# Kernel optimization log

Hardware: AMD Instinct MI355X
Metric: run time of the kernel (lower is better)

Reference implementation:

```python
import jax, jax.numpy as jnp
import numpy as np
from math import sqrt

B, T, E, W, H = 4, 512, 1024, 64, 16
DK = E // H


def _make_position_mask(T, W):
    # mask[s, w, t] = 1 iff token s is the w-th neighbor in the window around t
    t = np.arange(T)[None, :]            # [1, T]
    w = np.arange(W)[:, None]            # [W, 1]
    idx = np.clip(t - W // 2 + w, 0, T - 1)  # [W, T] source index per (w, t)
    mask = np.zeros((T, W, T), dtype=np.float32)
    mask[idx, np.arange(W)[:, None], np.arange(T)[None, :]] = 1.0
    return jnp.asarray(mask)


def setup_inputs() -> dict:
    key = jax.random.key(0)
    ks = jax.random.split(key, 7)
    s = 1.0 / sqrt(E)
    return {
        "x": jax.random.normal(ks[0], (B, T, E), jnp.float32),
        "position_mask": _make_position_mask(T, W),
        "Wq": jax.random.normal(ks[1], (E, E), jnp.float32) * s,
        "bq": jnp.zeros((E,), jnp.float32),
        "Wv": jax.random.normal(ks[2], (E, E), jnp.float32) * s,
        "bv": jnp.zeros((E,), jnp.float32),
        "Wo": jax.random.normal(ks[3], (E, E), jnp.float32) * s,
        "bo": jnp.zeros((E,), jnp.float32),
    }


def reference(x, position_mask, Wq, bq, Wv, bv, Wo, bo):
    # gather window neighbors: attend_inputs[b,t,w,e] = sum_s x[b,s,e] * mask[s,w,t]
    attend = jnp.einsum('bse,swt->btwe', x, position_mask)  # [B,T,W,E]

    # NOTE: original splits E as (d_k, H) with d_k-major (view(..., d_k, H))
    q = (x @ Wq + bq).reshape(B, T, DK, H)                    # [B,T,DK,H]
    q = q.transpose(0, 3, 1, 2)                               # [B,H,T,DK]
    k = (attend @ Wq + bq).reshape(B, T, W, DK, H)            # key uses query_transform (as in source)
    k = k.transpose(0, 4, 1, 2, 3)                            # [B,H,T,W,DK]
    v = (attend @ Wv + bv).reshape(B, T, W, DK, H)
    v = v.transpose(0, 4, 1, 2, 3)                            # [B,H,T,W,DK]

    scores = jnp.einsum('bhtd,bhtwd->bhtw', q, k) / sqrt(E)   # scale by sqrt(E), as in source
    probs = jax.nn.softmax(scores, axis=-1)                   # softmax over window W
    out = jnp.einsum('bhtw,bhtwd->bhtd', probs, v)            # [B,H,T,DK]
    out = out.transpose(0, 2, 1, 3).reshape(B, T, E)          # merge (H, DK) H-major, as in source reshape
    return out @ Wo + bo
```

## Files before the change

### kernel.cpp

```cpp
#include <hip/hip_runtime.h>
#include <hip/hip_bf16.h>

typedef __attribute__((ext_vector_type(8))) short short8;
typedef __attribute__((ext_vector_type(4))) float f32x4;
typedef __attribute__((ext_vector_type(4))) unsigned int uint4v;

constexpr int NB = 4, NT = 512, NE = 1024, NW = 64, NH = 16, NDK = 64;
constexpr int NBT = NB * NT;
constexpr int TT = 32;
constexpr int WIN = TT + 64;

__device__ inline short f2bf(float f) {
    __hip_bfloat16 h = __float2bfloat16(f);
    return __builtin_bit_cast(short, h);
}
__device__ inline float bf2f(short s) {
    unsigned u = ((unsigned)(unsigned short)s) << 16;
    return __builtin_bit_cast(float, u);
}
__device__ inline float blo(unsigned u) { return __builtin_bit_cast(float, u << 16); }
__device__ inline float bhi(unsigned u) { return __builtin_bit_cast(float, u & 0xffff0000u); }

__global__ __launch_bounds__(256) void cast_x_kernel(const float* __restrict__ X,
                                                     short* __restrict__ Xb) {
    size_t idx = (size_t)blockIdx.x * 256 + threadIdx.x;
    const float4* p = (const float4*)(X + idx * 8);
    float4 a = p[0], b = p[1];
    short8 v;
    v[0] = f2bf(a.x); v[1] = f2bf(a.y); v[2] = f2bf(a.z); v[3] = f2bf(a.w);
    v[4] = f2bf(b.x); v[5] = f2bf(b.y); v[6] = f2bf(b.z); v[7] = f2bf(b.w);
    *(short8*)(Xb + idx * 8) = v;
}

__global__ __launch_bounds__(256) void transpose_w_kernel(const float* __restrict__ W0,
                                                          const float* __restrict__ W1,
                                                          const float* __restrict__ W2,
                                                          short* __restrict__ WTall) {
    const float* W = blockIdx.z == 0 ? W0 : (blockIdx.z == 1 ? W1 : W2);
    const bool perm = blockIdx.z < 2;
    short* WT = WTall + (size_t)blockIdx.z * NE * NE;

    __shared__ float tile[64][65];
    const int e0 = blockIdx.y * 64, j0 = blockIdx.x * 64;
    const int el = threadIdx.x & 63, grp = threadIdx.x >> 6;
    for (int i = grp; i < 64; i += 4)
        tile[i][el] = W[(size_t)(e0 + i) * NE + j0 + el];
    __syncthreads();
    for (int it = grp; it < 64; it += 4) {
        int j = j0 + it;
        int jp = perm ? ((j & 15) * 64 + (j >> 4)) : j;
        WT[(size_t)jp * NE + e0 + el] = f2bf(tile[el][it]);
    }
}

template <bool PERM_BIAS, bool OUT_BF16>
__global__ __launch_bounds__(256) void mfma_gemm_kernel(const short* __restrict__ X,
                                                        const short* __restrict__ WT,
                                                        const float* __restrict__ bias,
                                                        void* __restrict__ outv) {
    __shared__ short As[64 * 64];
    __shared__ short Bs[64 * 64];
    const int tid = threadIdx.x;
    const int lane = tid & 63, wid = tid >> 6;

    int bid = blockIdx.y * 16 + blockIdx.x;
    int swz = (bid & 7) * 64 + (bid >> 3);
    const int r0 = (swz >> 4) * 64;
    const int c0 = (swz & 15) * 64;
    const int wr = (wid >> 1) * 32, wc = (wid & 1) * 32;

    f32x4 acc[2][2];
#pragma unroll
    for (int m = 0; m < 2; m++)
#pragma unroll
        for (int n = 0; n < 2; n++) acc[m][n] = (f32x4){0.f, 0.f, 0.f, 0.f};

    short8 pfA[2], pfB[2];
    auto load_tiles = [&](int k0) {
#pragma unroll
        for (int rd = 0; rd < 2; rd++) {
            int slot = rd * 4096 + tid * 16;
            int row  = slot >> 7;
            int cp   = (slot >> 4) & 7;
            int c    = cp ^ (row & 7);
            pfA[rd] = *(const short8*)(X  + (size_t)(r0 + row) * NE + k0 + c * 8);
            pfB[rd] = *(const short8*)(WT + (size_t)(c0 + row) * NE + k0 + c * 8);
        }
    };

    load_tiles(0);
    for (int k0 = 0; k0 < NE; k0 += 64) {
        __syncthreads();
#pragma unroll
        for (int rd = 0; rd < 2; rd++) {
            int slot = rd * 4096 + tid * 16;
            *(short8*)((char*)As + slot) = pfA[rd];
            *(short8*)((char*)Bs + slot) = pfB[rd];
        }
        __syncthreads();
        if (k0 + 64 < NE) load_tiles(k0 + 64);

#pragma unroll
        for (int kk = 0; kk < 2; kk++) {
            short8 af[2], bf[2];
            const int cidx = kk * 4 + (lane >> 4);
#pragma unroll
            for (int m = 0; m < 2; m++) {
                int row = wr + m * 16 + (lane & 15);
                af[m] = *(const short8*)((char*)As + row * 128 + ((cidx ^ (row & 7)) * 16));
            }
#pragma unroll
            for (int n = 0; n < 2; n++) {
                int row = wc + n * 16 + (lane & 15);
                bf[n] = *(const short8*)((char*)Bs + row * 128 + ((cidx ^ (row & 7)) * 16));
            }
#pragma unroll
            for (int m = 0; m < 2; m++)
#pragma unroll
                for (int n = 0; n < 2; n++)
                    acc[m][n] = __builtin_amdgcn_mfma_f32_16x16x32_bf16(af[m], bf[n], acc[m][n], 0, 0, 0);
        }
    }

    short* outS = (short*)outv;
    float* outF = (float*)outv;
#pragma unroll
    for (int m = 0; m < 2; m++)
#pragma unroll
        for (int n = 0; n < 2; n++) {
            int col  = c0 + wc + n * 16 + (lane & 15);
            int bsrc = PERM_BIAS ? ((col & 63) * 16 + (col >> 6)) : col;
            float bb = bias[bsrc];
#pragma unroll
            for (int r = 0; r < 4; r++) {
                int row = r0 + wr + m * 16 + (lane >> 4) * 4 + r;
                float val = acc[m][n][r] + bb;
                if (OUT_BF16) outS[(size_t)row * NE + col] = f2bf(val);
                else          outF[(size_t)row * NE + col] = val;
            }
        }
}

__global__ __launch_bounds__(256) void attn_kernel(const short* __restrict__ Y,
                                                   const short* __restrict__ Z,
                                                   short* __restrict__ M) {
    __shared__ short KS[WIN][66];
    __shared__ short VS[WIN][66];
    __shared__ short SCb[TT][66];
    __shared__ float RED[TT][16];

    const int t0 = blockIdx.x * TT;
    const int h  = blockIdx.y;
    const int b  = blockIdx.z;
    const int tid = threadIdx.x;
    const int tl  = tid & (TT - 1);
    const int oct = tid >> 5;

    for (int idx = tid; idx < WIN * 8; idx += 256) {
        int row = idx >> 3, c = idx & 7;
        int ts = t0 - 32 + row;
        ts = ts < 0 ? 0 : (ts > NT - 1 ? NT - 1 : ts);
        size_t base = ((size_t)b * NT + ts) * NE + h * 64 + c * 8;
        uint4v ku = __builtin_bit_cast(uint4v, *(const short8*)(Y + base));
        uint4v vu = __builtin_bit_cast(uint4v, *(const short8*)(Z + base));
        unsigned* kd = (unsigned*)&KS[row][c * 8];
        unsigned* vd = (unsigned*)&VS[row][c * 8];
        kd[0] = ku[0]; kd[1] = ku[1]; kd[2] = ku[2]; kd[3] = ku[3];
        vd[0] = vu[0]; vd[1] = vu[1]; vd[2] = vu[2]; vd[3] = vu[3];
    }
    __syncthreads();

    float q[64];
    {
        const unsigned* Qr = (const unsigned*)&KS[tl + 32][0];
#pragma unroll
        for (int k2 = 0; k2 < 32; k2++) {
            unsigned u = Qr[k2];
            q[2 * k2]     = blo(u);
            q[2 * k2 + 1] = bhi(u);
        }
    }

    float sv[8];
#pragma unroll
    for (int wi = 0; wi < 8; wi++) {
        int w = oct * 8 + wi;
        const unsigned* Kr = (const unsigned*)&KS[tl + w][0];
        float acc = 0.f;
#pragma unroll
        for (int k2 = 0; k2 < 32; k2++) {
            unsigned u = Kr[k2];
            acc += q[2 * k2] * blo(u) + q[2 * k2 + 1] * bhi(u);
        }
        sv[wi] = acc * 0.03125f;
    }

    float lmax = sv[0];
#pragma unroll
    for (int wi = 1; wi < 8; wi++) lmax = fmaxf(lmax, sv[wi]);
    RED[tl][oct] = lmax;
    __syncthreads();
    float gmax = RED[tl][0];
#pragma unroll
    for (int i = 1; i < 8; i++) gmax = fmaxf(gmax, RED[tl][i]);
    float lsum = 0.f;
#pragma unroll
    for (int wi = 0; wi < 8; wi++) {
        float e = __expf(sv[wi] - gmax);
        SCb[tl][oct * 8 + wi] = f2bf(e);
        lsum += e;
    }
    RED[tl][8 + oct] = lsum;
    __syncthreads();
    float gsum = RED[tl][8];
#pragma unroll
    for (int i = 9; i < 16; i++) gsum += RED[tl][i];

    float oacc[8];
#pragma unroll
    for (int j = 0; j < 8; j++) oacc[j] = 0.f;
    for (int w = 0; w < NW; w++) {
        float p = bf2f(SCb[tl][w]);
        const unsigned* Vr = (const unsigned*)&VS[tl + w][oct * 8];
#pragma unroll
        for (int j2 = 0; j2 < 4; j2++) {
            unsigned u = Vr[j2];
            oacc[2 * j2]     += p * blo(u);
            oacc[2 * j2 + 1] += p * bhi(u);
        }
    }

    float inv = 1.0f / gsum;
    short8 ov;
#pragma unroll
    for (int j = 0; j < 8; j++) ov[j] = f2bf(oacc[j] * inv);
    size_t orow = ((size_t)b * NT + t0 + tl) * NE + h * 64 + oct * 8;
    *(short8*)(M + orow) = ov;
}

extern "C" void kernel_launch(void* const* d_in, const int* in_sizes, int n_in,
                              void* d_out, int out_size, void* d_ws, size_t ws_size,
                              hipStream_t stream) {
    const float* x  = (const float*)d_in[0];
    const float* Wq = (const float*)d_in[2];
    const float* bq = (const float*)d_in[3];
    const float* Wv = (const float*)d_in[4];
    const float* bv = (const float*)d_in[5];
    const float* Wo = (const float*)d_in[6];
    const float* bo = (const float*)d_in[7];
    float* outp = (float*)d_out;

    char* wsb = (char*)d_ws;
    short* Xb  = (short*)(wsb);
    short* WTa = (short*)(wsb + (4u << 20));
    short* Yb  = (short*)(wsb + (10u << 20));
    short* Zb  = (short*)(wsb + (14u << 20));
    short* Mb  = (short*)(wsb + (18u << 20));
    short* WTq = WTa;
    short* WTv = WTa + (size_t)NE * NE;
    short* WTo = WTv + (size_t)NE * NE;

    cast_x_kernel<<<dim3(NBT * NE / (256 * 8)), 256, 0, stream>>>(x, Xb);
    transpose_w_kernel<<<dim3(16, 16, 3), 256, 0, stream>>>(Wq, Wv, Wo, WTa);

    dim3 gg(NE / 64, NBT / 64);
    mfma_gemm_kernel<true,  true ><<<gg, 256, 0, stream>>>(Xb, WTq, bq, Yb);
    mfma_gemm_kernel<true,  true ><<<gg, 256, 0, stream>>>(Xb, WTv, bv, Zb);

    attn_kernel<<<dim3(NT / TT, NH, NB), 256, 0, stream>>>(Yb, Zb, Mb);

    mfma_gemm_kernel<false, false><<<gg, 256, 0, stream>>>(Mb, WTo, bo, (void*)outp);
}
```

Baseline: 174.6 us.

## Fuse Q and V projections into one GEMM and enlarge GEMM tiles

```diff
diff --git a/kernel.cpp b/kernel.cpp
--- a/kernel.cpp
+++ b/kernel.cpp
@@ -53,37 +53,48 @@
     }
 }
 
-template <bool PERM_BIAS, bool OUT_BF16>
+template <int BM, int BN, int LOG_GX, bool PERM_BIAS, bool OUT_BF16, bool DUAL>
 __global__ __launch_bounds__(256) void mfma_gemm_kernel(const short* __restrict__ X,
                                                         const short* __restrict__ WT,
-                                                        const float* __restrict__ bias,
-                                                        void* __restrict__ outv) {
-    __shared__ short As[64 * 64];
-    __shared__ short Bs[64 * 64];
+                                                        const float* __restrict__ bias0,
+                                                        const float* __restrict__ bias1,
+                                                        void* __restrict__ out0,
+                                                        void* __restrict__ out1) {
+    constexpr int MR = BM / 32, NR = BN / 32;
+    constexpr int RDA = BM / 32, RDB = BN / 32;
+
+    __shared__ short As[BM * 64];
+    __shared__ short Bs[BN * 64];
     const int tid = threadIdx.x;
     const int lane = tid & 63, wid = tid >> 6;
 
-    int bid = blockIdx.y * 16 + blockIdx.x;
-    int swz = (bid & 7) * 64 + (bid >> 3);
-    const int r0 = (swz >> 4) * 64;
-    const int c0 = (swz & 15) * 64;
-    const int wr = (wid >> 1) * 32, wc = (wid & 1) * 32;
-
-    f32x4 acc[2][2];
-#pragma unroll
-    for (int m = 0; m < 2; m++)
-#pragma unroll
-        for (int n = 0; n < 2; n++) acc[m][n] = (f32x4){0.f, 0.f, 0.f, 0.f};
-
-    short8 pfA[2], pfB[2];
+    const int nwg = (1 << LOG_GX) * gridDim.y;
+    const int bid = blockIdx.y * (1 << LOG_GX) + blockIdx.x;
+    const int swz = (bid & 7) * (nwg >> 3) + (bid >> 3);
+    const int r0 = (swz >> LOG_GX) * BM;
+    const int c0 = (swz & ((1 << LOG_GX) - 1)) * BN;
+    const int wr = (wid >> 1) * (BM / 2), wc = (wid & 1) * (BN / 2);
+
+    f32x4 acc[MR][NR];
+#pragma unroll
+    for (int m = 0; m < MR; m++)
+#pragma unroll
+        for (int n = 0; n < NR; n++) acc[m][n] = (f32x4){0.f, 0.f, 0.f, 0.f};
+
+    short8 pfA[RDA], pfB[RDB];
     auto load_tiles = [&](int k0) {
 #pragma unroll
-        for (int rd = 0; rd < 2; rd++) {
+        for (int rd = 0; rd < RDA; rd++) {
             int slot = rd * 4096 + tid * 16;
             int row  = slot >> 7;
-            int cp   = (slot >> 4) & 7;
-            int c    = cp ^ (row & 7);
-            pfA[rd] = *(const short8*)(X  + (size_t)(r0 + row) * NE + k0 + c * 8);
+            int c    = ((slot >> 4) & 7) ^ (row & 7);
+            pfA[rd] = *(const short8*)(X + (size_t)(r0 + row) * NE + k0 + c * 8);
+        }
+#pragma unroll
+        for (int rd = 0; rd < RDB; rd++) {
+            int slot = rd * 4096 + tid * 16;
+            int row  = slot >> 7;
+            int c    = ((slot >> 4) & 7) ^ (row & 7);
             pfB[rd] = *(const short8*)(WT + (size_t)(c0 + row) * NE + k0 + c * 8);
         }
     };
@@ -92,51 +103,55 @@
     for (int k0 = 0; k0 < NE; k0 += 64) {
         __syncthreads();
 #pragma unroll
-        for (int rd = 0; rd < 2; rd++) {
-            int slot = rd * 4096 + tid * 16;
-            *(short8*)((char*)As + slot) = pfA[rd];
-            *(short8*)((char*)Bs + slot) = pfB[rd];
-        }
+        for (int rd = 0; rd < RDA; rd++)
+            *(short8*)((char*)As + rd * 4096 + tid * 16) = pfA[rd];
+#pragma unroll
+        for (int rd = 0; rd < RDB; rd++)
+            *(short8*)((char*)Bs + rd * 4096 + tid * 16) = pfB[rd];
         __syncthreads();
         if (k0 + 64 < NE) load_tiles(k0 + 64);
 
 #pragma unroll
         for (int kk = 0; kk < 2; kk++) {
-            short8 af[2], bf[2];
+            short8 af[MR], bf[NR];
             const int cidx = kk * 4 + (lane >> 4);
 #pragma unroll
-            for (int m = 0; m < 2; m++) {
+            for (int m = 0; m < MR; m++) {
                 int row = wr + m * 16 + (lane & 15);
                 af[m] = *(const short8*)((char*)As + row * 128 + ((cidx ^ (row & 7)) * 16));
             }
 #pragma unroll
-            for (int n = 0; n < 2; n++) {
+            for (int n = 0; n < NR; n++) {
                 int row = wc + n * 16 + (lane & 15);
                 bf[n] = *(const short8*)((char*)Bs + row * 128 + ((cidx ^ (row & 7)) * 16));
             }
 #pragma unroll
-            for (int m = 0; m < 2; m++)
-#pragma unroll
-                for (int n = 0; n < 2; n++)
+            for (int m = 0; m < MR; m++)
+#pragma unroll
+                for (int n = 0; n < NR; n++)
                     acc[m][n] = __builtin_amdgcn_mfma_f32_16x16x32_bf16(af[m], bf[n], acc[m][n], 0, 0, 0);
         }
     }
 
+    const float* bias = bias0;
+    void* outv = out0;
+    int cbase = c0;
+    if (DUAL && c0 >= NE) { bias = bias1; outv = out1; cbase = c0 - NE; }
     short* outS = (short*)outv;
     float* outF = (float*)outv;
 #pragma unroll
-    for (int m = 0; m < 2; m++)
-#pragma unroll
-        for (int n = 0; n < 2; n++) {
-            int col  = c0 + wc + n * 16 + (lane & 15);
-            int bsrc = PERM_BIAS ? ((col & 63) * 16 + (col >> 6)) : col;
+    for (int m = 0; m < MR; m++)
+#pragma unroll
+        for (int n = 0; n < NR; n++) {
+            int lc   = cbase + wc + n * 16 + (lane & 15);
+            int bsrc = PERM_BIAS ? ((lc & 63) * 16 + (lc >> 6)) : lc;
             float bb = bias[bsrc];
 #pragma unroll
             for (int r = 0; r < 4; r++) {
                 int row = r0 + wr + m * 16 + (lane >> 4) * 4 + r;
                 float val = acc[m][n][r] + bb;
-                if (OUT_BF16) outS[(size_t)row * NE + col] = f2bf(val);
-                else          outF[(size_t)row * NE + col] = val;
+                if (OUT_BF16) outS[(size_t)row * NE + lc] = f2bf(val);
+                else          outF[(size_t)row * NE + lc] = val;
             }
         }
 }
@@ -256,18 +271,16 @@
     short* Yb  = (short*)(wsb + (10u << 20));
     short* Zb  = (short*)(wsb + (14u << 20));
     short* Mb  = (short*)(wsb + (18u << 20));
-    short* WTq = WTa;
-    short* WTv = WTa + (size_t)NE * NE;
-    short* WTo = WTv + (size_t)NE * NE;
+    short* WTo = WTa + 2 * (size_t)NE * NE;
 
     cast_x_kernel<<<dim3(NBT * NE / (256 * 8)), 256, 0, stream>>>(x, Xb);
     transpose_w_kernel<<<dim3(16, 16, 3), 256, 0, stream>>>(Wq, Wv, Wo, WTa);
 
-    dim3 gg(NE / 64, NBT / 64);
-    mfma_gemm_kernel<true,  true ><<<gg, 256, 0, stream>>>(Xb, WTq, bq, Yb);
-    mfma_gemm_kernel<true,  true ><<<gg, 256, 0, stream>>>(Xb, WTv, bv, Zb);
+    mfma_gemm_kernel<128, 128, 4, true, true, true>
+        <<<dim3(2 * NE / 128, NBT / 128), 256, 0, stream>>>(Xb, WTa, bq, bv, Yb, Zb);
 
     attn_kernel<<<dim3(NT / TT, NH, NB), 256, 0, stream>>>(Yb, Zb, Mb);
 
-    mfma_gemm_kernel<false, false><<<gg, 256, 0, stream>>>(Mb, WTo, bo, (void*)outp);
-}
+    mfma_gemm_kernel<64, 128, 3, false, false, false>
+        <<<dim3(NE / 128, NBT / 64), 256, 0, stream>>>(Mb, WTo, bo, nullptr, (void*)outp, nullptr);
+}
```

Result: faster. 168.8 us (-3.3%).

## Fuse all stages into one persistent cooperative kernel with grid barriers

Applied to the files above, without the earlier changes.

```diff
diff --git a/kernel.cpp b/kernel.cpp
--- a/kernel.cpp
+++ b/kernel.cpp
@@ -3,239 +3,326 @@
 
 typedef __attribute__((ext_vector_type(8))) short short8;
 typedef __attribute__((ext_vector_type(4))) float f32x4;
-typedef __attribute__((ext_vector_type(4))) unsigned int uint4v;
-
-constexpr int NB = 4, NT = 512, NE = 1024, NW = 64, NH = 16, NDK = 64;
-constexpr int NBT = NB * NT;
+
+constexpr int NT = 512, NE = 1024, NW = 64, NH = 16;
+constexpr int NBT = 2048;
 constexpr int TT = 32;
 constexpr int WIN = TT + 64;
+constexpr int GRID = 256, THREADS = 512;
 
 __device__ inline short f2bf(float f) {
     __hip_bfloat16 h = __float2bfloat16(f);
     return __builtin_bit_cast(short, h);
 }
-__device__ inline float bf2f(short s) {
-    unsigned u = ((unsigned)(unsigned short)s) << 16;
-    return __builtin_bit_cast(float, u);
-}
 __device__ inline float blo(unsigned u) { return __builtin_bit_cast(float, u << 16); }
 __device__ inline float bhi(unsigned u) { return __builtin_bit_cast(float, u & 0xffff0000u); }
 
-__global__ __launch_bounds__(256) void cast_x_kernel(const float* __restrict__ X,
-                                                     short* __restrict__ Xb) {
-    size_t idx = (size_t)blockIdx.x * 256 + threadIdx.x;
-    const float4* p = (const float4*)(X + idx * 8);
-    float4 a = p[0], b = p[1];
-    short8 v;
-    v[0] = f2bf(a.x); v[1] = f2bf(a.y); v[2] = f2bf(a.z); v[3] = f2bf(a.w);
-    v[4] = f2bf(b.x); v[5] = f2bf(b.y); v[6] = f2bf(b.z); v[7] = f2bf(b.w);
-    *(short8*)(Xb + idx * 8) = v;
+__device__ inline void gsync(unsigned* cnt, int slot) {
+    __syncthreads();
+    if (threadIdx.x == 0) {
+        __threadfence();
+        atomicAdd(&cnt[slot], 1u);
+        while (__hip_atomic_load(&cnt[slot], __ATOMIC_RELAXED,
+                                 __HIP_MEMORY_SCOPE_AGENT) < (unsigned)GRID) {}
+        __threadfence();
+    }
+    __syncthreads();
 }
 
-__global__ __launch_bounds__(256) void transpose_w_kernel(const float* __restrict__ W0,
-                                                          const float* __restrict__ W1,
-                                                          const float* __restrict__ W2,
-                                                          short* __restrict__ WTall) {
-    const float* W = blockIdx.z == 0 ? W0 : (blockIdx.z == 1 ? W1 : W2);
-    const bool perm = blockIdx.z < 2;
-    short* WT = WTall + (size_t)blockIdx.z * NE * NE;
-
-    __shared__ float tile[64][65];
-    const int e0 = blockIdx.y * 64, j0 = blockIdx.x * 64;
-    const int el = threadIdx.x & 63, grp = threadIdx.x >> 6;
-    for (int i = grp; i < 64; i += 4)
-        tile[i][el] = W[(size_t)(e0 + i) * NE + j0 + el];
-    __syncthreads();
-    for (int it = grp; it < 64; it += 4) {
-        int j = j0 + it;
-        int jp = perm ? ((j & 15) * 64 + (j >> 4)) : j;
-        WT[(size_t)jp * NE + e0 + el] = f2bf(tile[el][it]);
-    }
-}
-
-template <bool PERM_BIAS, bool OUT_BF16>
-__global__ __launch_bounds__(256) void mfma_gemm_kernel(const short* __restrict__ X,
-                                                        const short* __restrict__ WT,
-                                                        const float* __restrict__ bias,
-                                                        void* __restrict__ outv) {
-    __shared__ short As[64 * 64];
-    __shared__ short Bs[64 * 64];
+__global__ __launch_bounds__(THREADS)
+void mega_kernel(const float* __restrict__ x,
+                 const float* __restrict__ Wq, const float* __restrict__ bq,
+                 const float* __restrict__ Wv, const float* __restrict__ bv,
+                 const float* __restrict__ Wo, const float* __restrict__ bo,
+                 float* __restrict__ outp,
+                 short* __restrict__ Xb, short* __restrict__ WTa,
+                 short* __restrict__ Yb, short* __restrict__ Zb,
+                 short* __restrict__ Mb, unsigned* __restrict__ cnt) {
+    __shared__ __align__(16) char arena[64 * 1024];
     const int tid = threadIdx.x;
+    const int bid = blockIdx.x;
     const int lane = tid & 63, wid = tid >> 6;
 
-    int bid = blockIdx.y * 16 + blockIdx.x;
-    int swz = (bid & 7) * 64 + (bid >> 3);
-    const int r0 = (swz >> 4) * 64;
-    const int c0 = (swz & 15) * 64;
-    const int wr = (wid >> 1) * 32, wc = (wid & 1) * 32;
-
-    f32x4 acc[2][2];
-#pragma unroll
-    for (int m = 0; m < 2; m++)
-#pragma unroll
-        for (int n = 0; n < 2; n++) acc[m][n] = (f32x4){0.f, 0.f, 0.f, 0.f};
-
-    short8 pfA[2], pfB[2];
-    auto load_tiles = [&](int k0) {
-#pragma unroll
-        for (int rd = 0; rd < 2; rd++) {
-            int slot = rd * 4096 + tid * 16;
-            int row  = slot >> 7;
-            int cp   = (slot >> 4) & 7;
-            int c    = cp ^ (row & 7);
-            pfA[rd] = *(const short8*)(X  + (size_t)(r0 + row) * NE + k0 + c * 8);
-            pfB[rd] = *(const short8*)(WT + (size_t)(c0 + row) * NE + k0 + c * 8);
-        }
-    };
-
-    load_tiles(0);
-    for (int k0 = 0; k0 < NE; k0 += 64) {
-        __syncthreads();
-#pragma unroll
-        for (int rd = 0; rd < 2; rd++) {
-            int slot = rd * 4096 + tid * 16;
-            *(short8*)((char*)As + slot) = pfA[rd];
-            *(short8*)((char*)Bs + slot) = pfB[rd];
-        }
-        __syncthreads();
-        if (k0 + 64 < NE) load_tiles(k0 + 64);
-
-#pragma unroll
-        for (int kk = 0; kk < 2; kk++) {
-            short8 af[2], bf[2];
-            const int cidx = kk * 4 + (lane >> 4);
-#pragma unroll
-            for (int m = 0; m < 2; m++) {
-                int row = wr + m * 16 + (lane & 15);
-                af[m] = *(const short8*)((char*)As + row * 128 + ((cidx ^ (row & 7)) * 16));
-            }
+    {
+        const int gid = bid * THREADS + tid;
+#pragma unroll
+        for (int it = 0; it < 2; it++) {
+            size_t base = ((size_t)gid * 2 + it) * 8;
+            const float4* p = (const float4*)(x + base);
+            float4 a = p[0], b = p[1];
+            short8 v;
+            v[0] = f2bf(a.x); v[1] = f2bf(a.y); v[2] = f2bf(a.z); v[3] = f2bf(a.w);
+            v[4] = f2bf(b.x); v[5] = f2bf(b.y); v[6] = f2bf(b.z); v[7] = f2bf(b.w);
+            *(short8*)(Xb + base) = v;
+        }
+        float (*tile)[65] = (float(*)[65])arena;
+        const int rl = tid >> 3, cl = (tid & 7) * 8;
+        for (int it = 0; it < 3; it++) {
+            int tile_id = bid * 3 + it;
+            int mi = tile_id >> 8;
+            int rem = tile_id & 255;
+            int e0 = (rem >> 4) * 64, j0 = (rem & 15) * 64;
+            const float* W = mi == 0 ? Wq : (mi == 1 ? Wv : Wo);
+            short* WT = WTa + (size_t)mi * NE * NE;
+            __syncthreads();
+            const float4* src = (const float4*)(W + (size_t)(e0 + rl) * NE + j0 + cl);
+            float4 a = src[0], b = src[1];
+            tile[rl][cl + 0] = a.x; tile[rl][cl + 1] = a.y;
+            tile[rl][cl + 2] = a.z; tile[rl][cl + 3] = a.w;
+            tile[rl][cl + 4] = b.x; tile[rl][cl + 5] = b.y;
+            tile[rl][cl + 6] = b.z; tile[rl][cl + 7] = b.w;
+            __syncthreads();
+            int jg = j0 + rl;
+            int jp = (mi < 2) ? ((jg & 15) * 64 + (jg >> 4)) : jg;
+            short8 ov;
+#pragma unroll
+            for (int j = 0; j < 8; j++) ov[j] = f2bf(tile[cl + j][rl]);
+            *(short8*)(WT + (size_t)jp * NE + e0 + cl) = ov;
+        }
+    }
+    gsync(cnt, 0);
+
+    {
+        short* As = (short*)arena;
+        short* Bs = (short*)(arena + 16384);
+        const int xcd = bid & 7, idx = bid >> 3;
+        const int c0 = (((xcd << 1) | (idx & 1))) * 128;
+        const int r0 = (idx >> 1) * 128;
+        const int wr = (wid & 1) * 64, wc = (wid >> 1) * 32;
+
+        f32x4 acc[4][2];
+#pragma unroll
+        for (int m = 0; m < 4; m++)
+#pragma unroll
+            for (int n = 0; n < 2; n++) acc[m][n] = (f32x4){0.f, 0.f, 0.f, 0.f};
+
+        short8 pfA[2], pfB[2];
+        auto load_tiles = [&](int k0) {
+#pragma unroll
+            for (int rd = 0; rd < 2; rd++) {
+                int slot = rd * 8192 + tid * 16;
+                int row = slot >> 7;
+                int c = ((slot >> 4) & 7) ^ (row & 7);
+                pfA[rd] = *(const short8*)(Xb  + (size_t)(r0 + row) * NE + k0 + c * 8);
+                pfB[rd] = *(const short8*)(WTa + (size_t)(c0 + row) * NE + k0 + c * 8);
+            }
+        };
+        load_tiles(0);
+        for (int k0 = 0; k0 < NE; k0 += 64) {
+            __syncthreads();
+#pragma unroll
+            for (int rd = 0; rd < 2; rd++) {
+                *(short8*)(As + (rd * 8192 + tid * 16) / 2) = pfA[rd];
+                *(short8*)(Bs + (rd * 8192 + tid * 16) / 2) = pfB[rd];
+            }
+            __syncthreads();
+            if (k0 + 64 < NE) load_tiles(k0 + 64);
+#pragma unroll
+            for (int kk = 0; kk < 2; kk++) {
+                short8 af[4], bf[2];
+                const int cidx = kk * 4 + (lane >> 4);
+#pragma unroll
+                for (int m = 0; m < 4; m++) {
+                    int row = wr + m * 16 + (lane & 15);
+                    af[m] = *(const short8*)((char*)As + row * 128 + ((cidx ^ (row & 7)) * 16));
+                }
+#pragma unroll
+                for (int n = 0; n < 2; n++) {
+                    int row = wc + n * 16 + (lane & 15);
+                    bf[n] = *(const short8*)((char*)Bs + row * 128 + ((cidx ^ (row & 7)) * 16));
+                }
+#pragma unroll
+                for (int m = 0; m < 4; m++)
+#pragma unroll
+                    for (int n = 0; n < 2; n++)
+                        acc[m][n] = __builtin_amdgcn_mfma_f32_16x16x32_bf16(af[m], bf[n], acc[m][n], 0, 0, 0);
+            }
+        }
+        const bool isZ = (c0 >= NE);
+        short* outT = isZ ? Zb : Yb;
+        const float* bias = isZ ? bv : bq;
+        const int cb = c0 - (isZ ? NE : 0);
+#pragma unroll
+        for (int m = 0; m < 4; m++)
 #pragma unroll
             for (int n = 0; n < 2; n++) {
-                int row = wc + n * 16 + (lane & 15);
-                bf[n] = *(const short8*)((char*)Bs + row * 128 + ((cidx ^ (row & 7)) * 16));
-            }
-#pragma unroll
-            for (int m = 0; m < 2; m++)
-#pragma unroll
-                for (int n = 0; n < 2; n++)
-                    acc[m][n] = __builtin_amdgcn_mfma_f32_16x16x32_bf16(af[m], bf[n], acc[m][n], 0, 0, 0);
-        }
-    }
-
-    short* outS = (short*)outv;
-    float* outF = (float*)outv;
-#pragma unroll
-    for (int m = 0; m < 2; m++)
-#pragma unroll
-        for (int n = 0; n < 2; n++) {
-            int col  = c0 + wc + n * 16 + (lane & 15);
-            int bsrc = PERM_BIAS ? ((col & 63) * 16 + (col >> 6)) : col;
-            float bb = bias[bsrc];
-#pragma unroll
-            for (int r = 0; r < 4; r++) {
-                int row = r0 + wr + m * 16 + (lane >> 4) * 4 + r;
-                float val = acc[m][n][r] + bb;
-                if (OUT_BF16) outS[(size_t)row * NE + col] = f2bf(val);
-                else          outF[(size_t)row * NE + col] = val;
-            }
-        }
-}
-
-__global__ __launch_bounds__(256) void attn_kernel(const short* __restrict__ Y,
-                                                   const short* __restrict__ Z,
-                                                   short* __restrict__ M) {
-    __shared__ short KS[WIN][66];
-    __shared__ short VS[WIN][66];
-    __shared__ short SCb[TT][66];
-    __shared__ float RED[TT][16];
-
-    const int t0 = blockIdx.x * TT;
-    const int h  = blockIdx.y;
-    const int b  = blockIdx.z;
-    const int tid = threadIdx.x;
-    const int tl  = tid & (TT - 1);
-    const int oct = tid >> 5;
-
-    for (int idx = tid; idx < WIN * 8; idx += 256) {
-        int row = idx >> 3, c = idx & 7;
-        int ts = t0 - 32 + row;
-        ts = ts < 0 ? 0 : (ts > NT - 1 ? NT - 1 : ts);
-        size_t base = ((size_t)b * NT + ts) * NE + h * 64 + c * 8;
-        uint4v ku = __builtin_bit_cast(uint4v, *(const short8*)(Y + base));
-        uint4v vu = __builtin_bit_cast(uint4v, *(const short8*)(Z + base));
-        unsigned* kd = (unsigned*)&KS[row][c * 8];
-        unsigned* vd = (unsigned*)&VS[row][c * 8];
-        kd[0] = ku[0]; kd[1] = ku[1]; kd[2] = ku[2]; kd[3] = ku[3];
-        vd[0] = vu[0]; vd[1] = vu[1]; vd[2] = vu[2]; vd[3] = vu[3];
-    }
-    __syncthreads();
-
-    float q[64];
+                int lc = cb + wc + n * 16 + (lane & 15);
+                float bb = bias[(lc & 63) * 16 + (lc >> 6)];
+#pragma unroll
+                for (int r = 0; r < 4; r++) {
+                    int row = r0 + wr + m * 16 + (lane >> 4) * 4 + r;
+                    outT[(size_t)row * NE + lc] = f2bf(acc[m][n][r] + bb);
+                }
+            }
+    }
+    gsync(cnt, 1);
+
     {
-        const unsigned* Qr = (const unsigned*)&KS[tl + 32][0];
-#pragma unroll
-        for (int k2 = 0; k2 < 32; k2++) {
-            unsigned u = Qr[k2];
-            q[2 * k2]     = blo(u);
-            q[2 * k2 + 1] = bhi(u);
-        }
-    }
-
-    float sv[8];
-#pragma unroll
-    for (int wi = 0; wi < 8; wi++) {
-        int w = oct * 8 + wi;
-        const unsigned* Kr = (const unsigned*)&KS[tl + w][0];
-        float acc = 0.f;
-#pragma unroll
-        for (int k2 = 0; k2 < 32; k2++) {
-            unsigned u = Kr[k2];
-            acc += q[2 * k2] * blo(u) + q[2 * k2 + 1] * bhi(u);
-        }
-        sv[wi] = acc * 0.03125f;
-    }
-
-    float lmax = sv[0];
-#pragma unroll
-    for (int wi = 1; wi < 8; wi++) lmax = fmaxf(lmax, sv[wi]);
-    RED[tl][oct] = lmax;
-    __syncthreads();
-    float gmax = RED[tl][0];
-#pragma unroll
-    for (int i = 1; i < 8; i++) gmax = fmaxf(gmax, RED[tl][i]);
-    float lsum = 0.f;
-#pragma unroll
-    for (int wi = 0; wi < 8; wi++) {
-        float e = __expf(sv[wi] - gmax);
-        SCb[tl][oct * 8 + wi] = f2bf(e);
-        lsum += e;
-    }
-    RED[tl][8 + oct] = lsum;
-    __syncthreads();
-    float gsum = RED[tl][8];
-#pragma unroll
-    for (int i = 9; i < 16; i++) gsum += RED[tl][i];
-
-    float oacc[8];
-#pragma unroll
-    for (int j = 0; j < 8; j++) oacc[j] = 0.f;
-    for (int w = 0; w < NW; w++) {
-        float p = bf2f(SCb[tl][w]);
-        const unsigned* Vr = (const unsigned*)&VS[tl + w][oct * 8];
-#pragma unroll
-        for (int j2 = 0; j2 < 4; j2++) {
-            unsigned u = Vr[j2];
-            oacc[2 * j2]     += p * blo(u);
-            oacc[2 * j2 + 1] += p * bhi(u);
-        }
-    }
-
-    float inv = 1.0f / gsum;
-    short8 ov;
-#pragma unroll
-    for (int j = 0; j < 8; j++) ov[j] = f2bf(oacc[j] * inv);
-    size_t orow = ((size_t)b * NT + t0 + tl) * NE + h * 64 + oct * 8;
-    *(short8*)(M + orow) = ov;
+        const int h2 = tid >> 8;
+        const int ltid = tid & 255;
+        const int tl = ltid & (TT - 1);
+        const int oct = ltid >> 5;
+        char* hb = arena + h2 * 32768;
+        short (*KS)[66]  = (short(*)[66])(hb);
+        short (*VS)[66]  = (short(*)[66])(hb + 12672);
+        short (*SCb)[66] = (short(*)[66])(hb + 25344);
+        float (*RED)[16] = (float(*)[16])(hb + 29568);
+
+        for (int round = 0; round < 2; round++) {
+            __syncthreads();
+            int u = bid * 4 + round * 2 + h2;
+            int t0 = (u & 15) * TT;
+            int h  = (u >> 4) & 15;
+            int b  = u >> 8;
+
+            for (int idx2 = ltid; idx2 < WIN * 8; idx2 += 256) {
+                int row = idx2 >> 3, c = idx2 & 7;
+                int ts = t0 - 32 + row;
+                ts = ts < 0 ? 0 : (ts > NT - 1 ? NT - 1 : ts);
+                size_t base = ((size_t)b * NT + ts) * NE + h * 64 + c * 8;
+                *(short8*)&KS[row][c * 8] = *(const short8*)(Yb + base);
+                *(short8*)&VS[row][c * 8] = *(const short8*)(Zb + base);
+            }
+            __syncthreads();
+
+            float q[64];
+            {
+                const unsigned* Qr = (const unsigned*)&KS[tl + 32][0];
+#pragma unroll
+                for (int k2 = 0; k2 < 32; k2++) {
+                    unsigned uu = Qr[k2];
+                    q[2 * k2] = blo(uu); q[2 * k2 + 1] = bhi(uu);
+                }
+            }
+            float sv[8];
+#pragma unroll
+            for (int wi = 0; wi < 8; wi++) {
+                const unsigned* Kr = (const unsigned*)&KS[tl + oct * 8 + wi][0];
+                float a2 = 0.f;
+#pragma unroll
+                for (int k2 = 0; k2 < 32; k2++) {
+                    unsigned uu = Kr[k2];
+                    a2 += q[2 * k2] * blo(uu) + q[2 * k2 + 1] * bhi(uu);
+                }
+                sv[wi] = a2 * 0.03125f;
+            }
+            float lmax = sv[0];
+#pragma unroll
+            for (int wi = 1; wi < 8; wi++) lmax = fmaxf(lmax, sv[wi]);
+            RED[tl][oct] = lmax;
+            __syncthreads();
+            float gmax = RED[tl][0];
+#pragma unroll
+            for (int i = 1; i < 8; i++) gmax = fmaxf(gmax, RED[tl][i]);
+            float lsum = 0.f;
+#pragma unroll
+            for (int wi = 0; wi < 8; wi++) {
+                float e = __expf(sv[wi] - gmax);
+                SCb[tl][oct * 8 + wi] = f2bf(e);
+                lsum += e;
+            }
+            RED[tl][8 + oct] = lsum;
+            __syncthreads();
+            float gsum = RED[tl][8];
+#pragma unroll
+            for (int i = 9; i < 16; i++) gsum += RED[tl][i];
+
+            float oacc[8];
+#pragma unroll
+            for (int j = 0; j < 8; j++) oacc[j] = 0.f;
+            for (int w = 0; w < NW; w++) {
+                float p = blo((unsigned)(unsigned short)SCb[tl][w]);
+                const unsigned* Vr = (const unsigned*)&VS[tl + w][oct * 8];
+#pragma unroll
+                for (int j2 = 0; j2 < 4; j2++) {
+                    unsigned uu = Vr[j2];
+                    oacc[2 * j2]     += p * blo(uu);
+                    oacc[2 * j2 + 1] += p * bhi(uu);
+                }
+            }
+            float inv = 1.0f / gsum;
+            short8 ov;
+#pragma unroll
+            for (int j = 0; j < 8; j++) ov[j] = f2bf(oacc[j] * inv);
+            *(short8*)(Mb + ((size_t)b * NT + t0 + tl) * NE + h * 64 + oct * 8) = ov;
+        }
+    }
+    gsync(cnt, 2);
+
+    {
+        short* As = (short*)arena;
+        short* Bs = (short*)(arena + 16384);
+        const short* WTo = WTa + 2 * (size_t)NE * NE;
+        const int xcd = bid & 7, idx = bid >> 3;
+        const int c0 = (((xcd << 1) | (idx & 1))) * 64;
+        const int r0 = (idx >> 1) * 128;
+        const int wr = (wid & 3) * 32, wc = (wid >> 2) * 32;
+
+        f32x4 acc[2][2];
+#pragma unroll
+        for (int m = 0; m < 2; m++)
+#pragma unroll
+            for (int n = 0; n < 2; n++) acc[m][n] = (f32x4){0.f, 0.f, 0.f, 0.f};
+
+        short8 pfA[2], pfB;
+        auto load_tiles = [&](int k0) {
+#pragma unroll
+            for (int rd = 0; rd < 2; rd++) {
+                int slot = rd * 8192 + tid * 16;
+                int row = slot >> 7;
+                int c = ((slot >> 4) & 7) ^ (row & 7);
+                pfA[rd] = *(const short8*)(Mb + (size_t)(r0 + row) * NE + k0 + c * 8);
+            }
+            {
+                int slot = tid * 16;
+                int row = slot >> 7;
+                int c = ((slot >> 4) & 7) ^ (row & 7);
+                pfB = *(const short8*)(WTo + (size_t)(c0 + row) * NE + k0 + c * 8);
+            }
+        };
+        load_tiles(0);
+        for (int k0 = 0; k0 < NE; k0 += 64) {
+            __syncthreads();
+#pragma unroll
+            for (int rd = 0; rd < 2; rd++)
+                *(short8*)(As + (rd * 8192 + tid * 16) / 2) = pfA[rd];
+            *(short8*)(Bs + (tid * 16) / 2) = pfB;
+            __syncthreads();
+            if (k0 + 64 < NE) load_tiles(k0 + 64);
+#pragma unroll
+            for (int kk = 0; kk < 2; kk++) {
+                short8 af[2], bf[2];
+                const int cidx = kk * 4 + (lane >> 4);
+#pragma unroll
+                for (int m = 0; m < 2; m++) {
+                    int row = wr + m * 16 + (lane & 15);
+                    af[m] = *(const short8*)((char*)As + row * 128 + ((cidx ^ (row & 7)) * 16));
+                }
+#pragma unroll
+                for (int n = 0; n < 2; n++) {
+                    int row = wc + n * 16 + (lane & 15);
+                    bf[n] = *(const short8*)((char*)Bs + row * 128 + ((cidx ^ (row & 7)) * 16));
+                }
+#pragma unroll
+                for (int m = 0; m < 2; m++)
+#pragma unroll
+                    for (int n = 0; n < 2; n++)
+                        acc[m][n] = __builtin_amdgcn_mfma_f32_16x16x32_bf16(af[m], bf[n], acc[m][n], 0, 0, 0);
+            }
+        }
+#pragma unroll
+        for (int m = 0; m < 2; m++)
+#pragma unroll
+            for (int n = 0; n < 2; n++) {
+                int col = c0 + wc + n * 16 + (lane & 15);
+                float bb = bo[col];
+#pragma unroll
+                for (int r = 0; r < 4; r++) {
+                    int row = r0 + wr + m * 16 + (lane >> 4) * 4 + r;
+                    outp[(size_t)row * NE + col] = acc[m][n][r] + bb;
+                }
+            }
+    }
 }
 
 extern "C" void kernel_launch(void* const* d_in, const int* in_sizes, int n_in,
@@ -256,18 +343,12 @@
     short* Yb  = (short*)(wsb + (10u << 20));
     short* Zb  = (short*)(wsb + (14u << 20));
     short* Mb  = (short*)(wsb + (18u << 20));
-    short* WTq = WTa;
-    short* WTv = WTa + (size_t)NE * NE;
-    short* WTo = WTv + (size_t)NE * NE;
-
-    cast_x_kernel<<<dim3(NBT * NE / (256 * 8)), 256, 0, stream>>>(x, Xb);
-    transpose_w_kernel<<<dim3(16, 16, 3), 256, 0, stream>>>(Wq, Wv, Wo, WTa);
-
-    dim3 gg(NE / 64, NBT / 64);
-    mfma_gemm_kernel<true,  true ><<<gg, 256, 0, stream>>>(Xb, WTq, bq, Yb);
-    mfma_gemm_kernel<true,  true ><<<gg, 256, 0, stream>>>(Xb, WTv, bv, Zb);
-
-    attn_kernel<<<dim3(NT / TT, NH, NB), 256, 0, stream>>>(Yb, Zb, Mb);
-
-    mfma_gemm_kernel<false, false><<<gg, 256, 0, stream>>>(Mb, WTo, bo, (void*)outp);
+    unsigned* cnt = (unsigned*)(wsb + (24u << 20));
+
+    hipMemsetAsync(cnt, 0, 4 * sizeof(unsigned), stream);
+
+    void* args[] = {&x, &Wq, &bq, &Wv, &bv, &Wo, &bo, &outp,
+                    &Xb, &WTa, &Yb, &Zb, &Mb, &cnt};
+    hipLaunchCooperativeKernel((void*)mega_kernel, dim3(GRID), dim3(THREADS),
+                               args, 0, stream);
 }
```

After: 255.8 us. +46.5%, slower.
